# Kernel optimization log

Hardware: AMD Instinct MI355X
Metric: run time of the kernel (lower is better)

## Reference

```python
import jax, jax.numpy as jnp
import numpy as np

EMB = 1024
HEADS = 8
HEAD_DIM = EMB // HEADS


def setup_inputs() -> dict:
    key = jax.random.key(0)
    ks = jax.random.split(key, 11)
    B, S = 4, 2048
    scale = 1.0 / np.sqrt(EMB)
    inp = {
        "query": jax.random.normal(ks[0], (B, S, EMB), jnp.float32),
        "key": jax.random.normal(ks[1], (B, S, EMB), jnp.float32),
        "value": jax.random.normal(ks[2], (B, S, EMB), jnp.float32),
        "Wq": jax.random.normal(ks[3], (EMB, EMB), jnp.float32) * scale,
        "bq": jnp.zeros((EMB,), jnp.float32),
        "Wk": jax.random.normal(ks[4], (EMB, EMB), jnp.float32) * scale,
        "bk": jnp.zeros((EMB,), jnp.float32),
        "Wv": jax.random.normal(ks[5], (EMB, EMB), jnp.float32) * scale,
        "bv": jnp.zeros((EMB,), jnp.float32),
        "Wo": jax.random.normal(ks[6], (EMB, EMB), jnp.float32) * scale,
        "bo": jnp.zeros((EMB,), jnp.float32),
    }
    return inp


def _split_heads(x):
    B, S, _ = x.shape
    return x.reshape(B, S, HEADS, HEAD_DIM).transpose(0, 2, 1, 3)  # [B,H,S,D]


def reference(query, key, value, Wq, bq, Wk, bk, Wv, bv, Wo, bo):
    Q = _split_heads(query @ Wq.T + bq)
    K = _split_heads(key @ Wk.T + bk)
    V = _split_heads(value @ Wv.T + bv)
    # [B,H,S,S] attention scores, scaled by sqrt(head_dim)
    scores = jnp.einsum("bhqd,bhkd->bhqk", Q, K) / jnp.sqrt(
        jnp.asarray(HEAD_DIM, Q.dtype)
    )
    attention = jax.nn.softmax(scores, axis=-1)
    # dropout is identity in eval mode
    x = jnp.einsum("bhqk,bhkd->bhqd", attention, V)
    B, H, S, D = x.shape
    x = x.transpose(0, 2, 1, 3).reshape(B, S, EMB)
    x = x @ Wo.T + bo
    return (x, attention)
```

## Files before the change

kernel.cpp:

```cpp
#include <hip/hip_runtime.h>
#include <hip/hip_bf16.h>
#include <math.h>

#define BB 4
#define SS 2048
#define EMB 1024
#define HH 8
#define DD 128

typedef __attribute__((ext_vector_type(8))) short bf16x8;
typedef __attribute__((ext_vector_type(4))) float f32x4;

__device__ __forceinline__ unsigned short f2bf(float f) {
    unsigned u = __builtin_bit_cast(unsigned, f);
    u += 0x7FFFu + ((u >> 16) & 1u);
    return (unsigned short)(u >> 16);
}

__device__ __forceinline__ void gload_lds16(const void* g, void* l) {
    __builtin_amdgcn_global_load_lds(
        (const __attribute__((address_space(1))) unsigned int*)g,
        (__attribute__((address_space(3))) unsigned int*)l, 16, 0, 0);
}

__global__ void f2bf_kernel(const float* __restrict__ src,
                            unsigned short* __restrict__ dst, int n4) {
    int i = blockIdx.x * blockDim.x + threadIdx.x;
    int stride = gridDim.x * blockDim.x;
    for (; i < n4; i += stride) {
        float4 f = ((const float4*)src)[i];
        ushort4 o;
        o.x = f2bf(f.x); o.y = f2bf(f.y); o.z = f2bf(f.z); o.w = f2bf(f.w);
        ((ushort4*)dst)[i] = o;
    }
}

template <int MODE>
__global__ __launch_bounds__(256, 2)
void gemm_bt(const unsigned short* __restrict__ A,
             const unsigned short* __restrict__ Bw,
             const float* __restrict__ bias,
             void* __restrict__ Cout, float scale)
{
    __shared__ short As[128 * 32];
    __shared__ short Bs[128 * 32];
    const int K = 1024;
    const int m0 = blockIdx.x * 128, n0 = blockIdx.y * 128;
    const int t = threadIdx.x;
    const int lane = t & 63, w = t >> 6;
    const int wr = w >> 1, wc = w & 1;
    const int g = lane >> 4, li = lane & 15;
    f32x4 acc[4][4] = {};

    for (int k0 = 0; k0 < K; k0 += 32) {
        __syncthreads();
        #pragma unroll
        for (int i = 0; i < 2; ++i) {
            int idx = i * 256 + t;
            int row = idx >> 2, col = (idx & 3) * 8;
            gload_lds16(A  + (size_t)(m0 + row) * K + k0 + col, &As[idx * 8]);
            gload_lds16(Bw + (size_t)(n0 + row) * K + k0 + col, &Bs[idx * 8]);
        }
        __syncthreads();
        bf16x8 af[4], bfr[4];
        #pragma unroll
        for (int mi = 0; mi < 4; ++mi)
            af[mi] = *(const bf16x8*)&As[(wr * 64 + mi * 16 + li) * 32 + g * 8];
        #pragma unroll
        for (int ni = 0; ni < 4; ++ni)
            bfr[ni] = *(const bf16x8*)&Bs[(wc * 64 + ni * 16 + li) * 32 + g * 8];
        #pragma unroll
        for (int mi = 0; mi < 4; ++mi) {
            #pragma unroll
            for (int ni = 0; ni < 4; ++ni)
                acc[mi][ni] = __builtin_amdgcn_mfma_f32_16x16x32_bf16(
                    af[mi], bfr[ni], acc[mi][ni], 0, 0, 0);
        }
    }

    #pragma unroll
    for (int mi = 0; mi < 4; ++mi) {
        #pragma unroll
        for (int ni = 0; ni < 4; ++ni) {
            int n = n0 + wc * 64 + ni * 16 + li;
            float bv = bias[n];
            #pragma unroll
            for (int i = 0; i < 4; ++i) {
                int m = m0 + wr * 64 + mi * 16 + g * 4 + i;
                float v = acc[mi][ni][i] + bv;
                if (MODE == 0) {
                    v *= scale;
                    int b = m >> 11, s = m & 2047, h = n >> 7, d = n & 127;
                    ((unsigned short*)Cout)[((((size_t)b * HH + h) * SS + s) << 7) + d] = f2bf(v);
                } else {
                    ((float*)Cout)[(size_t)m * EMB + n] = v;
                }
            }
        }
    }
}

__global__ __launch_bounds__(256, 2)
void attn_kernel(const unsigned short* __restrict__ Qb,
                 const unsigned short* __restrict__ Kb,
                 const unsigned short* __restrict__ Vb,
                 float* __restrict__ attn,
                 unsigned short* __restrict__ Ob)
{
    __shared__ short Ks[64 * 128];
    __shared__ short Vt[128 * 64];
    __shared__ short Ps[4][16 * 68];

    const int t = threadIdx.x;
    const int lane = t & 63, w = t >> 6;
    const int g = lane >> 4, li = lane & 15;
    const int bh = blockIdx.y;
    const int q0 = blockIdx.x * 64 + w * 16;

    const unsigned short* Kbh = Kb + (size_t)bh * SS * DD;
    const unsigned short* Vbh = Vb + (size_t)bh * SS * DD;

    bf16x8 qf[4];
    {
        const unsigned short* qp = Qb + ((size_t)bh * SS + q0 + li) * DD + g * 8;
        #pragma unroll
        for (int kk = 0; kk < 4; ++kk) qf[kk] = *(const bf16x8*)(qp + kk * 32);
    }

    float m_i[4], l_i[4];
    #pragma unroll
    for (int i = 0; i < 4; ++i) { m_i[i] = -1e30f; l_i[i] = 0.f; }

    auto stageK = [&](int kt2, char* dst) {
        const char* ksrc = (const char*)(Kbh + kt2 * 64 * DD);
        #pragma unroll
        for (int i = 0; i < 4; ++i) {
            int lb = (i * 256 + t) * 16;
            int row = lb >> 8;
            gload_lds16(ksrc + (lb ^ ((row & 7) << 4)), dst + lb);
        }
    };

    stageK(0, (char*)Ks);
    for (int kt = 0; kt < 32; ++kt) {
        const char* cur = (kt & 1) ? (const char*)Vt : (const char*)Ks;
        char* nxt = (kt & 1) ? (char*)Ks : (char*)Vt;
        if (kt < 31) {
            stageK(kt + 1, nxt);
            asm volatile("s_waitcnt vmcnt(4)");
        } else {
            asm volatile("s_waitcnt vmcnt(0)");
        }
        __builtin_amdgcn_sched_barrier(0);
        __builtin_amdgcn_s_barrier();
        __builtin_amdgcn_sched_barrier(0);

        f32x4 sacc[4];
        #pragma unroll
        for (int kc = 0; kc < 4; ++kc) {
            f32x4 a = {0.f, 0.f, 0.f, 0.f};
            int row = kc * 16 + li;
            int sw = (row & 7) << 4;
            #pragma unroll
            for (int kk = 0; kk < 4; ++kk) {
                bf16x8 kf = *(const bf16x8*)(cur + row * 256 + ((kk * 64 + g * 16) ^ sw));
                a = __builtin_amdgcn_mfma_f32_16x16x32_bf16(qf[kk], kf, a, 0, 0, 0);
            }
            sacc[kc] = a;
        }
        #pragma unroll
        for (int i = 0; i < 4; ++i) {
            float tm = fmaxf(fmaxf(sacc[0][i], sacc[1][i]), fmaxf(sacc[2][i], sacc[3][i]));
            #pragma unroll
            for (int mk = 1; mk < 16; mk <<= 1) tm = fmaxf(tm, __shfl_xor(tm, mk, 64));
            float mn = fmaxf(m_i[i], tm);
            float ts = __builtin_amdgcn_exp2f(sacc[0][i] - mn) + __builtin_amdgcn_exp2f(sacc[1][i] - mn)
                     + __builtin_amdgcn_exp2f(sacc[2][i] - mn) + __builtin_amdgcn_exp2f(sacc[3][i] - mn);
            #pragma unroll
            for (int mk = 1; mk < 16; mk <<= 1) ts += __shfl_xor(ts, mk, 64);
            l_i[i] = l_i[i] * __builtin_amdgcn_exp2f(m_i[i] - mn) + ts;
            m_i[i] = mn;
        }
        __builtin_amdgcn_s_barrier();
        __builtin_amdgcn_sched_barrier(0);
    }

    float rl[4];
    #pragma unroll
    for (int i = 0; i < 4; ++i) rl[i] = 1.f / l_i[i];

    f32x4 O[8] = {};
    float* arow = attn + (size_t)bh * SS * SS;

    bf16x8 va[2], vbr[2];
    #pragma unroll
    for (int i = 0; i < 2; ++i) {
        int idx = i * 256 + t;
        int k0 = (idx >> 4) * 2, d0 = (idx & 15) * 8;
        va[i]  = *(const bf16x8*)(Vbh + k0 * DD + d0);
        vbr[i] = *(const bf16x8*)(Vbh + (k0 + 1) * DD + d0);
    }

    for (int kt = 0; kt < 32; ++kt) {
        __syncthreads();
        const char* ksrc = (const char*)(Kbh + kt * 64 * DD);
        #pragma unroll
        for (int i = 0; i < 4; ++i) {
            int lb = (i * 256 + t) * 16;
            int row = lb >> 8;
            gload_lds16(ksrc + (lb ^ ((row & 7) << 4)), (char*)Ks + lb);
        }
        #pragma unroll
        for (int i = 0; i < 2; ++i) {
            int idx = i * 256 + t;
            int kpair = idx >> 4, d0 = (idx & 15) * 8;
            #pragma unroll
            for (int j = 0; j < 8; ++j) {
                unsigned pk = (unsigned)(unsigned short)va[i][j]
                            | ((unsigned)(unsigned short)vbr[i][j] << 16);
                int d = d0 + j;
                int ba = (d * 128 + kpair * 4) ^ (((d >> 3) & 7) << 4);
                *(unsigned*)((char*)Vt + ba) = pk;
            }
        }
        __syncthreads();

        if (kt < 31) {
            const unsigned short* vn = Vbh + (kt + 1) * 64 * DD;
            #pragma unroll
            for (int i = 0; i < 2; ++i) {
                int idx = i * 256 + t;
                int k0 = (idx >> 4) * 2, d0 = (idx & 15) * 8;
                va[i]  = *(const bf16x8*)(vn + k0 * DD + d0);
                vbr[i] = *(const bf16x8*)(vn + (k0 + 1) * DD + d0);
            }
        }

        #pragma unroll
        for (int kc = 0; kc < 4; ++kc) {
            f32x4 a = {0.f, 0.f, 0.f, 0.f};
            int row = kc * 16 + li;
            int sw = (row & 7) << 4;
            #pragma unroll
            for (int kk = 0; kk < 4; ++kk) {
                bf16x8 kf = *(const bf16x8*)((const char*)Ks + row * 256 + ((kk * 64 + g * 16) ^ sw));
                a = __builtin_amdgcn_mfma_f32_16x16x32_bf16(qf[kk], kf, a, 0, 0, 0);
            }
            #pragma unroll
            for (int i = 0; i < 4; ++i) {
                float p = __builtin_amdgcn_exp2f(a[i] - m_i[i]) * rl[i];
                int qr = g * 4 + i;
                __builtin_nontemporal_store(p, &arow[(size_t)(q0 + qr) * SS + kt * 64 + kc * 16 + li]);
                Ps[w][qr * 68 + kc * 16 + li] = (short)f2bf(p);
            }
        }
        asm volatile("s_waitcnt lgkmcnt(0)" ::: "memory");
        __builtin_amdgcn_sched_barrier(0);

        bf16x8 pf0 = *(const bf16x8*)&Ps[w][li * 68 + g * 8];
        bf16x8 pf1 = *(const bf16x8*)&Ps[w][li * 68 + 32 + g * 8];
        #pragma unroll
        for (int dt = 0; dt < 8; ++dt) {
            int dr = dt * 16 + li;
            int vsw = ((dr >> 3) & 7) << 4;
            bf16x8 vf0 = *(const bf16x8*)((const char*)Vt + dr * 128 + ((g * 16) ^ vsw));
            bf16x8 vf1 = *(const bf16x8*)((const char*)Vt + dr * 128 + ((64 + g * 16) ^ vsw));
            O[dt] = __builtin_amdgcn_mfma_f32_16x16x32_bf16(pf0, vf0, O[dt], 0, 0, 0);
            O[dt] = __builtin_amdgcn_mfma_f32_16x16x32_bf16(pf1, vf1, O[dt], 0, 0, 0);
        }
    }

    const int b = bh >> 3, h = bh & 7;
    #pragma unroll
    for (int dt = 0; dt < 8; ++dt) {
        #pragma unroll
        for (int i = 0; i < 4; ++i) {
            size_t r = (size_t)b * SS + q0 + g * 4 + i;
            Ob[r * EMB + h * DD + dt * 16 + li] = f2bf(O[dt][i]);
        }
    }
}

extern "C" void kernel_launch(void* const* d_in, const int* in_sizes, int n_in,
                              void* d_out, int out_size, void* d_ws, size_t ws_size,
                              hipStream_t stream)
{
    const float* q  = (const float*)d_in[0];
    const float* k  = (const float*)d_in[1];
    const float* v  = (const float*)d_in[2];
    const float* Wq = (const float*)d_in[3];
    const float* bq = (const float*)d_in[4];
    const float* Wk = (const float*)d_in[5];
    const float* bk = (const float*)d_in[6];
    const float* Wv = (const float*)d_in[7];
    const float* bv = (const float*)d_in[8];
    const float* Wo = (const float*)d_in[9];
    const float* bo = (const float*)d_in[10];

    const size_t NX = (size_t)BB * SS * EMB;
    const size_t NW = (size_t)EMB * EMB;

    unsigned short* Qb = (unsigned short*)d_ws;
    unsigned short* Kb = Qb + NX;
    unsigned short* Vb = Kb + NX;
    unsigned short* Ob = Vb + NX;
    unsigned short* WB = Ob + NX;

    float* outx = (float*)d_out;
    float* attn = outx + NX;
    unsigned short* XB = (unsigned short*)attn;

    f2bf_kernel<<<2048, 256, 0, stream>>>(q, XB,          (int)(NX / 4));
    f2bf_kernel<<<2048, 256, 0, stream>>>(k, XB + NX,     (int)(NX / 4));
    f2bf_kernel<<<2048, 256, 0, stream>>>(v, XB + 2 * NX, (int)(NX / 4));
    f2bf_kernel<<<512, 256, 0, stream>>>(Wq, WB,          (int)(NW / 4));
    f2bf_kernel<<<512, 256, 0, stream>>>(Wk, WB + NW,     (int)(NW / 4));
    f2bf_kernel<<<512, 256, 0, stream>>>(Wv, WB + 2 * NW, (int)(NW / 4));
    f2bf_kernel<<<512, 256, 0, stream>>>(Wo, WB + 3 * NW, (int)(NW / 4));

    const float qscale = 1.4426950408889634f / sqrtf((float)DD);
    dim3 ggrid(64, 8);
    gemm_bt<0><<<ggrid, 256, 0, stream>>>(XB,          WB,          bq, Qb, qscale);
    gemm_bt<0><<<ggrid, 256, 0, stream>>>(XB + NX,     WB + NW,     bk, Kb, 1.f);
    gemm_bt<0><<<ggrid, 256, 0, stream>>>(XB + 2 * NX, WB + 2 * NW, bv, Vb, 1.f);

    dim3 agrid(32, 32);
    attn_kernel<<<agrid, 256, 0, stream>>>(Qb, Kb, Vb, attn, Ob);

    gemm_bt<1><<<ggrid, 256, 0, stream>>>(Ob, WB + 3 * NW, bo, outx, 1.f);
}
```

Before: 403.2 us.

## Double-buffer GEMM and attention LDS tiles, batch conversion and QKV launches

The GEMM now double-buffers its A/B LDS tiles, so the next k-slice loads while MFMAs run on the current one. The attention pass-2 loop double-buffers the K and transposed-V tiles, with the V transpose scatter issued during the PV MFMAs. The seven conversion kernels become two batched launches, and the three QKV GEMMs become one launch with a z-dimension. This removes load stalls and launch gaps, at the cost of doubled LDS use, which may reduce occupancy in the attention kernel (about 68KB per block).

New measurement: 417.1 us. 3.5% more time.

```diff
diff --git a/kernel.cpp b/kernel.cpp
--- a/kernel.cpp
+++ b/kernel.cpp
@@ -23,27 +23,46 @@
         (__attribute__((address_space(3))) unsigned int*)l, 16, 0, 0);
 }
 
-__global__ void f2bf_kernel(const float* __restrict__ src,
-                            unsigned short* __restrict__ dst, int n4) {
+#define SB0 __builtin_amdgcn_sched_barrier(0)
+
+__global__ void f2bf3_kernel(const float* __restrict__ a, const float* __restrict__ b,
+                             const float* __restrict__ c, unsigned short* __restrict__ dst,
+                             int n4) {
+    const float* src = blockIdx.z == 0 ? a : (blockIdx.z == 1 ? b : c);
+    unsigned short* d = dst + (size_t)blockIdx.z * ((size_t)n4 * 4);
     int i = blockIdx.x * blockDim.x + threadIdx.x;
     int stride = gridDim.x * blockDim.x;
     for (; i < n4; i += stride) {
         float4 f = ((const float4*)src)[i];
         ushort4 o;
         o.x = f2bf(f.x); o.y = f2bf(f.y); o.z = f2bf(f.z); o.w = f2bf(f.w);
-        ((ushort4*)dst)[i] = o;
+        ((ushort4*)d)[i] = o;
+    }
+}
+
+__global__ void f2bf4_kernel(const float* __restrict__ a, const float* __restrict__ b,
+                             const float* __restrict__ c, const float* __restrict__ e,
+                             unsigned short* __restrict__ dst, int n4) {
+    const float* src = blockIdx.z == 0 ? a : (blockIdx.z == 1 ? b : (blockIdx.z == 2 ? c : e));
+    unsigned short* d = dst + (size_t)blockIdx.z * ((size_t)n4 * 4);
+    int i = blockIdx.x * blockDim.x + threadIdx.x;
+    int stride = gridDim.x * blockDim.x;
+    for (; i < n4; i += stride) {
+        float4 f = ((const float4*)src)[i];
+        ushort4 o;
+        o.x = f2bf(f.x); o.y = f2bf(f.y); o.z = f2bf(f.z); o.w = f2bf(f.w);
+        ((ushort4*)d)[i] = o;
     }
 }
 
 template <int MODE>
-__global__ __launch_bounds__(256, 2)
-void gemm_bt(const unsigned short* __restrict__ A,
-             const unsigned short* __restrict__ Bw,
-             const float* __restrict__ bias,
-             void* __restrict__ Cout, float scale)
-{
-    __shared__ short As[128 * 32];
-    __shared__ short Bs[128 * 32];
+__device__ __forceinline__ void gemm_core(const unsigned short* __restrict__ A,
+                                          const unsigned short* __restrict__ Bw,
+                                          const float* __restrict__ bias,
+                                          void* __restrict__ Cout, float scale)
+{
+    __shared__ short As[2][128 * 32];
+    __shared__ short Bs[2][128 * 32];
     const int K = 1024;
     const int m0 = blockIdx.x * 128, n0 = blockIdx.y * 128;
     const int t = threadIdx.x;
@@ -52,23 +71,34 @@
     const int g = lane >> 4, li = lane & 15;
     f32x4 acc[4][4] = {};
 
-    for (int k0 = 0; k0 < K; k0 += 32) {
-        __syncthreads();
+    auto stage = [&](int k0, int buf) {
         #pragma unroll
         for (int i = 0; i < 2; ++i) {
             int idx = i * 256 + t;
             int row = idx >> 2, col = (idx & 3) * 8;
-            gload_lds16(A  + (size_t)(m0 + row) * K + k0 + col, &As[idx * 8]);
-            gload_lds16(Bw + (size_t)(n0 + row) * K + k0 + col, &Bs[idx * 8]);
-        }
-        __syncthreads();
+            gload_lds16(A  + (size_t)(m0 + row) * K + k0 + col, &As[buf][idx * 8]);
+            gload_lds16(Bw + (size_t)(n0 + row) * K + k0 + col, &Bs[buf][idx * 8]);
+        }
+    };
+
+    stage(0, 0);
+    for (int ki = 0; ki < 32; ++ki) {
+        const int cur = ki & 1;
+        if (ki < 31) {
+            stage((ki + 1) * 32, cur ^ 1);
+            asm volatile("s_waitcnt vmcnt(4)" ::: "memory");
+        } else {
+            asm volatile("s_waitcnt vmcnt(0)" ::: "memory");
+        }
+        SB0; __builtin_amdgcn_s_barrier(); SB0;
+
         bf16x8 af[4], bfr[4];
         #pragma unroll
         for (int mi = 0; mi < 4; ++mi)
-            af[mi] = *(const bf16x8*)&As[(wr * 64 + mi * 16 + li) * 32 + g * 8];
+            af[mi] = *(const bf16x8*)&As[cur][(wr * 64 + mi * 16 + li) * 32 + g * 8];
         #pragma unroll
         for (int ni = 0; ni < 4; ++ni)
-            bfr[ni] = *(const bf16x8*)&Bs[(wc * 64 + ni * 16 + li) * 32 + g * 8];
+            bfr[ni] = *(const bf16x8*)&Bs[cur][(wc * 64 + ni * 16 + li) * 32 + g * 8];
         #pragma unroll
         for (int mi = 0; mi < 4; ++mi) {
             #pragma unroll
@@ -76,6 +106,8 @@
                 acc[mi][ni] = __builtin_amdgcn_mfma_f32_16x16x32_bf16(
                     af[mi], bfr[ni], acc[mi][ni], 0, 0, 0);
         }
+        asm volatile("s_waitcnt lgkmcnt(0)" ::: "memory");
+        SB0; __builtin_amdgcn_s_barrier(); SB0;
     }
 
     #pragma unroll
@@ -101,14 +133,33 @@
 }
 
 __global__ __launch_bounds__(256, 2)
+void gemm_qkv(const unsigned short* __restrict__ XB, const unsigned short* __restrict__ WB,
+              const float* __restrict__ bq, const float* __restrict__ bk,
+              const float* __restrict__ bv, unsigned short* __restrict__ QKVb, float qscale)
+{
+    const size_t NX = (size_t)BB * SS * EMB;
+    const size_t NW = (size_t)EMB * EMB;
+    const int z = blockIdx.z;
+    const float* bias = z == 0 ? bq : (z == 1 ? bk : bv);
+    gemm_core<0>(XB + z * NX, WB + z * NW, bias, QKVb + z * NX, z == 0 ? qscale : 1.f);
+}
+
+__global__ __launch_bounds__(256, 2)
+void gemm_out(const unsigned short* __restrict__ Ob, const unsigned short* __restrict__ Wo,
+              const float* __restrict__ bo, float* __restrict__ outx)
+{
+    gemm_core<1>(Ob, Wo, bo, outx, 1.f);
+}
+
+__global__ __launch_bounds__(256, 2)
 void attn_kernel(const unsigned short* __restrict__ Qb,
                  const unsigned short* __restrict__ Kb,
                  const unsigned short* __restrict__ Vb,
                  float* __restrict__ attn,
                  unsigned short* __restrict__ Ob)
 {
-    __shared__ short Ks[64 * 128];
-    __shared__ short Vt[128 * 64];
+    __shared__ short Ks2[2][64 * 128];
+    __shared__ short Vt2[2][128 * 64];
     __shared__ short Ps[4][16 * 68];
 
     const int t = threadIdx.x;
@@ -141,19 +192,16 @@
         }
     };
 
-    stageK(0, (char*)Ks);
+    stageK(0, (char*)Ks2[0]);
     for (int kt = 0; kt < 32; ++kt) {
-        const char* cur = (kt & 1) ? (const char*)Vt : (const char*)Ks;
-        char* nxt = (kt & 1) ? (char*)Ks : (char*)Vt;
+        const char* cur = (const char*)Ks2[kt & 1];
         if (kt < 31) {
-            stageK(kt + 1, nxt);
-            asm volatile("s_waitcnt vmcnt(4)");
+            stageK(kt + 1, (char*)Ks2[(kt & 1) ^ 1]);
+            asm volatile("s_waitcnt vmcnt(4)" ::: "memory");
         } else {
-            asm volatile("s_waitcnt vmcnt(0)");
-        }
-        __builtin_amdgcn_sched_barrier(0);
-        __builtin_amdgcn_s_barrier();
-        __builtin_amdgcn_sched_barrier(0);
+            asm volatile("s_waitcnt vmcnt(0)" ::: "memory");
+        }
+        SB0; __builtin_amdgcn_s_barrier(); SB0;
 
         f32x4 sacc[4];
         #pragma unroll
@@ -181,8 +229,7 @@
             l_i[i] = l_i[i] * __builtin_amdgcn_exp2f(m_i[i] - mn) + ts;
             m_i[i] = mn;
         }
-        __builtin_amdgcn_s_barrier();
-        __builtin_amdgcn_sched_barrier(0);
+        __builtin_amdgcn_s_barrier(); SB0;
     }
 
     float rl[4];
@@ -193,23 +240,17 @@
     float* arow = attn + (size_t)bh * SS * SS;
 
     bf16x8 va[2], vbr[2];
-    #pragma unroll
-    for (int i = 0; i < 2; ++i) {
-        int idx = i * 256 + t;
-        int k0 = (idx >> 4) * 2, d0 = (idx & 15) * 8;
-        va[i]  = *(const bf16x8*)(Vbh + k0 * DD + d0);
-        vbr[i] = *(const bf16x8*)(Vbh + (k0 + 1) * DD + d0);
-    }
-
-    for (int kt = 0; kt < 32; ++kt) {
-        __syncthreads();
-        const char* ksrc = (const char*)(Kbh + kt * 64 * DD);
-        #pragma unroll
-        for (int i = 0; i < 4; ++i) {
-            int lb = (i * 256 + t) * 16;
-            int row = lb >> 8;
-            gload_lds16(ksrc + (lb ^ ((row & 7) << 4)), (char*)Ks + lb);
-        }
+    auto issueV = [&](int kt2) {
+        const unsigned short* vn = Vbh + kt2 * 64 * DD;
+        #pragma unroll
+        for (int i = 0; i < 2; ++i) {
+            int idx = i * 256 + t;
+            int k0 = (idx >> 4) * 2, d0 = (idx & 15) * 8;
+            va[i]  = *(const bf16x8*)(vn + k0 * DD + d0);
+            vbr[i] = *(const bf16x8*)(vn + (k0 + 1) * DD + d0);
+        }
+    };
+    auto scatterV = [&](char* VtD) {
         #pragma unroll
         for (int i = 0; i < 2; ++i) {
             int idx = i * 256 + t;
@@ -220,22 +261,29 @@
                             | ((unsigned)(unsigned short)vbr[i][j] << 16);
                 int d = d0 + j;
                 int ba = (d * 128 + kpair * 4) ^ (((d >> 3) & 7) << 4);
-                *(unsigned*)((char*)Vt + ba) = pk;
-            }
-        }
-        __syncthreads();
-
+                *(unsigned*)(VtD + ba) = pk;
+            }
+        }
+    };
+
+    issueV(0);
+    stageK(0, (char*)Ks2[0]);
+    scatterV((char*)Vt2[0]);
+    asm volatile("s_waitcnt lgkmcnt(0)" ::: "memory");
+    SB0; __builtin_amdgcn_s_barrier(); SB0;
+
+    for (int kt = 0; kt < 32; ++kt) {
+        const int cur = kt & 1, nxt = cur ^ 1;
         if (kt < 31) {
-            const unsigned short* vn = Vbh + (kt + 1) * 64 * DD;
-            #pragma unroll
-            for (int i = 0; i < 2; ++i) {
-                int idx = i * 256 + t;
-                int k0 = (idx >> 4) * 2, d0 = (idx & 15) * 8;
-                va[i]  = *(const bf16x8*)(vn + k0 * DD + d0);
-                vbr[i] = *(const bf16x8*)(vn + (k0 + 1) * DD + d0);
-            }
-        }
-
+            issueV(kt + 1);
+            stageK(kt + 1, (char*)Ks2[nxt]);
+        }
+        if (kt == 0)      { asm volatile("s_waitcnt vmcnt(8)"  ::: "memory"); }
+        else if (kt < 31) { asm volatile("s_waitcnt vmcnt(24)" ::: "memory"); }
+        else              { asm volatile("s_waitcnt vmcnt(16)" ::: "memory"); }
+        SB0; __builtin_amdgcn_s_barrier(); SB0;
+
+        const char* KsC = (const char*)Ks2[cur];
         #pragma unroll
         for (int kc = 0; kc < 4; ++kc) {
             f32x4 a = {0.f, 0.f, 0.f, 0.f};
@@ -243,7 +291,7 @@
             int sw = (row & 7) << 4;
             #pragma unroll
             for (int kk = 0; kk < 4; ++kk) {
-                bf16x8 kf = *(const bf16x8*)((const char*)Ks + row * 256 + ((kk * 64 + g * 16) ^ sw));
+                bf16x8 kf = *(const bf16x8*)(KsC + row * 256 + ((kk * 64 + g * 16) ^ sw));
                 a = __builtin_amdgcn_mfma_f32_16x16x32_bf16(qf[kk], kf, a, 0, 0, 0);
             }
             #pragma unroll
@@ -255,19 +303,24 @@
             }
         }
         asm volatile("s_waitcnt lgkmcnt(0)" ::: "memory");
-        __builtin_amdgcn_sched_barrier(0);
-
+        SB0;
         bf16x8 pf0 = *(const bf16x8*)&Ps[w][li * 68 + g * 8];
         bf16x8 pf1 = *(const bf16x8*)&Ps[w][li * 68 + 32 + g * 8];
+
+        if (kt < 31) scatterV((char*)Vt2[nxt]);
+
+        const char* VtC = (const char*)Vt2[cur];
         #pragma unroll
         for (int dt = 0; dt < 8; ++dt) {
             int dr = dt * 16 + li;
             int vsw = ((dr >> 3) & 7) << 4;
-            bf16x8 vf0 = *(const bf16x8*)((const char*)Vt + dr * 128 + ((g * 16) ^ vsw));
-            bf16x8 vf1 = *(const bf16x8*)((const char*)Vt + dr * 128 + ((64 + g * 16) ^ vsw));
+            bf16x8 vf0 = *(const bf16x8*)(VtC + dr * 128 + ((g * 16) ^ vsw));
+            bf16x8 vf1 = *(const bf16x8*)(VtC + dr * 128 + ((64 + g * 16) ^ vsw));
             O[dt] = __builtin_amdgcn_mfma_f32_16x16x32_bf16(pf0, vf0, O[dt], 0, 0, 0);
             O[dt] = __builtin_amdgcn_mfma_f32_16x16x32_bf16(pf1, vf1, O[dt], 0, 0, 0);
         }
+        asm volatile("s_waitcnt lgkmcnt(0)" ::: "memory");
+        SB0; __builtin_amdgcn_s_barrier(); SB0;
     }
 
     const int b = bh >> 3, h = bh & 7;
@@ -301,31 +354,20 @@
     const size_t NW = (size_t)EMB * EMB;
 
     unsigned short* Qb = (unsigned short*)d_ws;
-    unsigned short* Kb = Qb + NX;
-    unsigned short* Vb = Kb + NX;
-    unsigned short* Ob = Vb + NX;
+    unsigned short* Ob = Qb + 3 * NX;
     unsigned short* WB = Ob + NX;
 
     float* outx = (float*)d_out;
     float* attn = outx + NX;
     unsigned short* XB = (unsigned short*)attn;
 
-    f2bf_kernel<<<2048, 256, 0, stream>>>(q, XB,          (int)(NX / 4));
-    f2bf_kernel<<<2048, 256, 0, stream>>>(k, XB + NX,     (int)(NX / 4));
-    f2bf_kernel<<<2048, 256, 0, stream>>>(v, XB + 2 * NX, (int)(NX / 4));
-    f2bf_kernel<<<512, 256, 0, stream>>>(Wq, WB,          (int)(NW / 4));
-    f2bf_kernel<<<512, 256, 0, stream>>>(Wk, WB + NW,     (int)(NW / 4));
-    f2bf_kernel<<<512, 256, 0, stream>>>(Wv, WB + 2 * NW, (int)(NW / 4));
-    f2bf_kernel<<<512, 256, 0, stream>>>(Wo, WB + 3 * NW, (int)(NW / 4));
+    f2bf3_kernel<<<dim3(1024, 1, 3), 256, 0, stream>>>(q, k, v, XB, (int)(NX / 4));
+    f2bf4_kernel<<<dim3(128, 1, 4), 256, 0, stream>>>(Wq, Wk, Wv, Wo, WB, (int)(NW / 4));
 
     const float qscale = 1.4426950408889634f / sqrtf((float)DD);
-    dim3 ggrid(64, 8);
-    gemm_bt<0><<<ggrid, 256, 0, stream>>>(XB,          WB,          bq, Qb, qscale);
-    gemm_bt<0><<<ggrid, 256, 0, stream>>>(XB + NX,     WB + NW,     bk, Kb, 1.f);
-    gemm_bt<0><<<ggrid, 256, 0, stream>>>(XB + 2 * NX, WB + 2 * NW, bv, Vb, 1.f);
-
-    dim3 agrid(32, 32);
-    attn_kernel<<<agrid, 256, 0, stream>>>(Qb, Kb, Vb, attn, Ob);
-
-    gemm_bt<1><<<ggrid, 256, 0, stream>>>(Ob, WB + 3 * NW, bo, outx, 1.f);
-}
+    gemm_qkv<<<dim3(64, 8, 3), 256, 0, stream>>>(XB, WB, bq, bk, bv, Qb, qscale);
+
+    attn_kernel<<<dim3(32, 32), 256, 0, stream>>>(Qb, Qb + NX, Qb + 2 * NX, attn, Ob);
+
+    gemm_out<<<dim3(64, 8), 256, 0, stream>>>(Ob, WB + 3 * NW, bo, outx);
+}
```
